# Performance work log

Hardware: AMD Instinct MI355X
Metric: run time of the kernel (lower is better)

## Reference

```python
import jax, jax.numpy as jnp
import numpy as np

NEG_INF = -1e20

def setup_inputs() -> dict:
    key = jax.random.key(0)
    kq, kk, kv, km = jax.random.split(key, 4)
    B, S, H, D = 2, 2048, 16, 64
    queries = jax.random.normal(kq, (B, S, H, D), dtype=jnp.float32)
    keys = jax.random.normal(kk, (B, S, H, D), dtype=jnp.float32)
    values = jax.random.normal(kv, (B, S, H, D), dtype=jnp.float32)
    mask = jax.random.randint(km, (B, 1, 1, S), 0, 2, dtype=jnp.int32)
    return {"queries": queries, "keys": keys, "values": values, "mask": mask}

def reference(queries, keys, values, mask):
    # scores: [B, H, Q, K]
    dk = keys.shape[-1]
    scores = jnp.einsum('bqhd,bkhd->bhqk', queries, keys) / jnp.sqrt(jnp.asarray(dk, queries.dtype))
    scores = jnp.where(mask == 0, jnp.asarray(NEG_INF, scores.dtype), scores)
    attn = jax.nn.softmax(scores, axis=-1)
    # dropout p=0.0 (eval): identity
    out = jnp.einsum('bhqv,bvhd->bqhd', attn, values)
    return out
```

## Files before the change

### kernel.cpp

```cpp
#include <hip/hip_runtime.h>
#include <hip/hip_bf16.h>

#define S_LEN 2048
#define NH 16
#define HD 64

typedef __attribute__((ext_vector_type(8))) __bf16 bf16x8;
typedef __attribute__((ext_vector_type(16))) float f32x16;

#define QSCALE 0.1803368801111204f

static __device__ __forceinline__ ushort f2bf(float f) {
    unsigned int u = __float_as_uint(f);
    u += 0x7fffu + ((u >> 16) & 1u);
    return (ushort)(u >> 16);
}

static __device__ __forceinline__ void gload16(const void* g, void* l) {
    __builtin_amdgcn_global_load_lds(
        (const __attribute__((address_space(1))) unsigned int*)g,
        (__attribute__((address_space(3))) unsigned int*)l, 16, 0, 0);
}
static __device__ __forceinline__ void gload4(const void* g, void* l) {
    __builtin_amdgcn_global_load_lds(
        (const __attribute__((address_space(1))) unsigned int*)g,
        (__attribute__((address_space(3))) unsigned int*)l, 4, 0, 0);
}

static __device__ __forceinline__ unsigned cvtpk_bf16(float lo, float hi) {
    unsigned r;
    asm("v_cvt_pk_bf16_f32 %0, %1, %2" : "=v"(r) : "v"(lo), "v"(hi));
    return r;
}
static __device__ __forceinline__ float exp2_fast(float x) {
    float r;
    asm("v_exp_f32 %0, %1" : "=v"(r) : "v"(x));
    return r;
}

__global__ __launch_bounds__(256) void prep_k_kernel(const float* __restrict__ in,
                                                     ushort* __restrict__ out) {
    unsigned t = blockIdx.x * 256u + threadIdx.x;
    unsigned o = t & 7u;
    unsigned s = (t >> 3) & 2047u;
    unsigned bh = t >> 14;
    unsigned b = bh >> 4, h = bh & 15u;
    const float* src = in + (((size_t)(b * S_LEN) + s) * NH + h) * HD + o * 8;
    float4 x = *(const float4*)src;
    float4 y = *(const float4*)(src + 4);
    union { ushort u[8]; uint4 q; } fu;
    fu.u[0] = f2bf(x.x); fu.u[1] = f2bf(x.y); fu.u[2] = f2bf(x.z); fu.u[3] = f2bf(x.w);
    fu.u[4] = f2bf(y.x); fu.u[5] = f2bf(y.y); fu.u[6] = f2bf(y.z); fu.u[7] = f2bf(y.w);
    unsigned kt = s >> 6, kh = (s >> 5) & 1u, kl = s & 31u;
    unsigned dchunk = o >> 1, ho = o & 1u;
    size_t ci = (((size_t)(bh * 32u + kt) * 2u + kh) * 4u + dchunk) * 64u + kl + 32u * ho;
    *(uint4*)(out + ci * 8u) = fu.q;
}

__global__ __launch_bounds__(256) void prep_v_kernel(const float* __restrict__ in,
                                                     ushort* __restrict__ out) {
    __shared__ float T[64][68];
    const unsigned tid = threadIdx.x;
    const unsigned kt = blockIdx.x, bh = blockIdx.y;
    const unsigned b = bh >> 4, h = bh & 15u;
#pragma unroll
    for (int i = 0; i < 4; ++i) {
        unsigned idx = tid + i * 256u;
        unsigned sl = idx >> 4, d4 = (idx & 15u) * 4u;
        float4 v = *(const float4*)(in + (((size_t)(b * S_LEN) + kt * 64u + sl) * NH + h) * HD + d4);
        *(float4*)&T[sl][d4] = v;
    }
    __syncthreads();
#pragma unroll
    for (int it = 0; it < 2; ++it) {
        unsigned ct = tid + it * 256u;
        unsigned l = ct & 63u, sub = ct >> 6;
        unsigned nt = sub & 1u, c = (sub >> 1) & 1u, kh = sub >> 2;
        unsigned d = (l & 31u) + 32u * nt;
        unsigned kb = kh * 32u + c * 16u + (l >> 5) * 8u;
        union { ushort u[8]; uint4 q; } fu;
#pragma unroll
        for (int j = 0; j < 8; ++j) fu.u[j] = f2bf(T[kb + j][d]);
        *(uint4*)(out + ((size_t)(bh * 32u + kt) * 8u + sub) * 512u + l * 8u) = fu.q;
    }
}

struct TileMem {
    ushort K[2][2][4096];
    ushort V[2][2][4096];
    int    mb[2][2][64];
};
struct CombMem {
    float ob[4][32][64];
    float lsb[4][64];
    float rls[4][32];
};
union SMemU { TileMem s; CombMem c; };

__global__ __launch_bounds__(512, 4) void attn_kernel(const float* __restrict__ Qp,
                                                      const ushort* __restrict__ Kws,
                                                      const ushort* __restrict__ Vws,
                                                      const int* __restrict__ maskp,
                                                      float* __restrict__ outp) {
    __shared__ __align__(16) SMemU sm;

    const unsigned tid = threadIdx.x;
    const unsigned wid = tid >> 6;
    const unsigned lane = tid & 63u;
    const unsigned l31 = lane & 31u;
    const unsigned hi = lane >> 5;
    const unsigned qsub = wid & 3u;
    const unsigned kgrp = wid >> 2;

    const unsigned bh = blockIdx.y;
    const unsigned b = bh >> 4, h = bh & 15u;
    const unsigned q0 = blockIdx.x * 128u + qsub * 32u;

    bf16x8 qf[4];
    {
        const float* qb = Qp + (((size_t)(b * S_LEN) + q0 + l31) * NH + h) * HD + hi * 8u;
#pragma unroll
        for (int dc = 0; dc < 4; ++dc) {
            float4 x = *(const float4*)(qb + dc * 16);
            float4 y = *(const float4*)(qb + dc * 16 + 4);
            union { ushort u[8]; bf16x8 v; } fu;
            fu.u[0] = f2bf(x.x * QSCALE); fu.u[1] = f2bf(x.y * QSCALE);
            fu.u[2] = f2bf(x.z * QSCALE); fu.u[3] = f2bf(x.w * QSCALE);
            fu.u[4] = f2bf(y.x * QSCALE); fu.u[5] = f2bf(y.y * QSCALE);
            fu.u[6] = f2bf(y.z * QSCALE); fu.u[7] = f2bf(y.w * QSCALE);
            qf[dc] = fu.v;
        }
    }

    f32x16 oacc0 = {0,0,0,0,0,0,0,0,0,0,0,0,0,0,0,0};
    f32x16 oacc1 = {0,0,0,0,0,0,0,0,0,0,0,0,0,0,0,0};
    float ls0 = 0.f, ls1 = 0.f, ls2 = 0.f, ls3 = 0.f;

    const char* kgp = (const char*)Kws + (size_t)bh * 262144u
                    + ((size_t)kgrp * 131072u) + (2u * qsub) * 1024u + lane * 16u;
    const char* vgp = (const char*)Vws + (size_t)bh * 262144u
                    + ((size_t)kgrp * 131072u) + (2u * qsub) * 1024u + lane * 16u;
    const int* mgp = maskp + (size_t)b * S_LEN + kgrp * 1024u + lane;

    ushort* klb = &sm.s.K[kgrp][0][2u * qsub * 512u];
    ushort* vlb = &sm.s.V[kgrp][0][2u * qsub * 512u];
    int*    mlb = &sm.s.mb[kgrp][0][0];
    const ushort* krd = &sm.s.K[kgrp][0][0];
    const ushort* vrd = &sm.s.V[kgrp][0][0];

#define STAGE(I, PB) do {                                                      \
    const size_t toff = (size_t)(I) * 8192u;                                   \
    gload16(kgp + toff,          klb + (PB) * 4096u);                          \
    gload16(kgp + toff + 1024u,  klb + (PB) * 4096u + 512u);                   \
    gload16(vgp + toff,          vlb + (PB) * 4096u);                          \
    gload16(vgp + toff + 1024u,  vlb + (PB) * 4096u + 512u);                   \
    if (qsub == 0) gload4(mgp + (I) * 64, mlb + (PB) * 64u);                   \
  } while (0)

    STAGE(0, 0u);
    asm volatile("s_waitcnt vmcnt(0)" ::: "memory");
    __syncthreads();

    unsigned pb = 0;
    for (int i = 0; i < 16; ++i) {
        if (i < 15) STAGE(i + 1, pb ^ 1u);
        const ushort* kr = krd + pb * 4096u;
        const ushort* vr = vrd + pb * 4096u;
        const int*    mr = mlb + pb * 64u;

#pragma unroll
        for (int kh = 0; kh < 2; ++kh) {
            bf16x8 kf[4];
#pragma unroll
            for (int dc = 0; dc < 4; ++dc)
                kf[dc] = *(const bf16x8*)&kr[(kh * 4 + dc) * 512u + lane * 8u];

            f32x16 s = {0,0,0,0,0,0,0,0,0,0,0,0,0,0,0,0};
            __builtin_amdgcn_s_setprio(1);
#pragma unroll
            for (int dc = 0; dc < 4; ++dc)
                s = __builtin_amdgcn_mfma_f32_32x32x16_bf16(kf[dc], qf[dc], s, 0, 0, 0);
            __builtin_amdgcn_s_setprio(0);

            float p[16];
#pragma unroll
            for (int r1 = 0; r1 < 4; ++r1) {
                int mv[4];
                *(int4*)mv = *(const int4*)&mr[kh * 32 + r1 * 8 + hi * 4];
#pragma unroll
                for (int r0 = 0; r0 < 4; ++r0) {
                    const int reg = r1 * 4 + r0;
                    float t = mv[r0] ? s[reg] : -1e30f;
                    p[reg] = exp2_fast(t);
                }
                ls0 += p[r1 * 4 + 0]; ls1 += p[r1 * 4 + 1];
                ls2 += p[r1 * 4 + 2]; ls3 += p[r1 * 4 + 3];
            }

#pragma unroll
            for (int c = 0; c < 2; ++c) {
                unsigned a0 = cvtpk_bf16(p[8 * c + 0], p[8 * c + 1]);
                unsigned a1 = cvtpk_bf16(p[8 * c + 2], p[8 * c + 3]);
                unsigned b0 = cvtpk_bf16(p[8 * c + 4], p[8 * c + 5]);
                unsigned b1 = cvtpk_bf16(p[8 * c + 6], p[8 * c + 7]);
                asm("v_permlane32_swap_b32 %0, %1" : "+v"(a0), "+v"(b0));
                asm("v_permlane32_swap_b32 %0, %1" : "+v"(a1), "+v"(b1));
                union { unsigned w[4]; bf16x8 v; } pa;
                pa.w[0] = a0; pa.w[1] = a1; pa.w[2] = b0; pa.w[3] = b1;
                bf16x8 vf0 = *(const bf16x8*)&vr[((kh * 2 + c) * 2 + 0) * 512u + lane * 8u];
                bf16x8 vf1 = *(const bf16x8*)&vr[((kh * 2 + c) * 2 + 1) * 512u + lane * 8u];
                __builtin_amdgcn_s_setprio(1);
                oacc0 = __builtin_amdgcn_mfma_f32_32x32x16_bf16(pa.v, vf0, oacc0, 0, 0, 0);
                oacc1 = __builtin_amdgcn_mfma_f32_32x32x16_bf16(pa.v, vf1, oacc1, 0, 0, 0);
                __builtin_amdgcn_s_setprio(0);
            }
        }
        asm volatile("s_waitcnt vmcnt(0)" ::: "memory");
        __syncthreads();
        pb ^= 1u;
    }
#undef STAGE

    float lsum = (ls0 + ls1) + (ls2 + ls3);
    lsum += __shfl_xor(lsum, 32);

    if (kgrp == 1) {
#pragma unroll
        for (int r = 0; r < 16; ++r) {
            sm.c.ob[qsub][r][lane]      = oacc0[r];
            sm.c.ob[qsub][16 + r][lane] = oacc1[r];
        }
        sm.c.lsb[qsub][lane] = lsum;
    }
    __syncthreads();
    if (kgrp == 0) {
        lsum += sm.c.lsb[qsub][lane];
#pragma unroll
        for (int r = 0; r < 16; ++r) {
            oacc0[r] += sm.c.ob[qsub][r][lane];
            oacc1[r] += sm.c.ob[qsub][16 + r][lane];
        }
        if (hi == 0) sm.c.rls[qsub][l31] = 1.0f / lsum;
#pragma unroll
        for (int r1 = 0; r1 < 4; ++r1) {
#pragma unroll
            for (int r0 = 0; r0 < 4; ++r0) {
                const int reg = r1 * 4 + r0;
                const unsigned q = r0 + 8u * r1 + 4u * hi;
                const float rr = sm.c.rls[qsub][q];
                float* ob = outp + (((size_t)(b * S_LEN) + q0 + q) * NH + h) * HD + l31;
                ob[0]  = oacc0[reg] * rr;
                ob[32] = oacc1[reg] * rr;
            }
        }
    }
}

extern "C" void kernel_launch(void* const* d_in, const int* in_sizes, int n_in,
                              void* d_out, int out_size, void* d_ws, size_t ws_size,
                              hipStream_t stream) {
    const float* Qp = (const float*)d_in[0];
    const float* Kp = (const float*)d_in[1];
    const float* Vp = (const float*)d_in[2];
    const int* maskp = (const int*)d_in[3];
    float* outp = (float*)d_out;

    ushort* Kws = (ushort*)d_ws;
    ushort* Vws = Kws + (size_t)2 * NH * S_LEN * HD;

    hipLaunchKernelGGL(prep_k_kernel, dim3(2048), dim3(256), 0, stream, Kp, Kws);
    hipLaunchKernelGGL(prep_v_kernel, dim3(32, 32), dim3(256), 0, stream, Vp, Vws);
    hipLaunchKernelGGL(attn_kernel, dim3(S_LEN / 128, 32), dim3(512), 0, stream,
                       Qp, Kws, Vws, maskp, outp);
}
```

Measured before the change: 64.16 us.

## Software-pipeline QK and softmax, compute row sums via MFMA, preload mask once

Restructures the inner loop so the second half-tile's QK MFMAs are issued between the first half's exp and its PV MFMAs, overlapping VALU work with matrix work. The row-sum accumulation moves from VALU adds plus a cross-lane shuffle to an extra MFMA against a vector of ones. The row sums then come out already in the output accumulator layout, so the shared-memory reciprocal broadcast is no longer needed. The whole mask row is loaded into LDS once instead of per tile. In exchange it adds 50% more PV MFMA work, raises accumulator register pressure, and sums bf16-rounded probabilities, which changes numerics slightly.

```diff
diff --git a/kernel.cpp b/kernel.cpp
--- a/kernel.cpp
+++ b/kernel.cpp
@@ -88,12 +88,11 @@
 struct TileMem {
     ushort K[2][2][4096];
     ushort V[2][2][4096];
-    int    mb[2][2][64];
+    int    mk[2][1024];
 };
 struct CombMem {
     float ob[4][32][64];
-    float lsb[4][64];
-    float rls[4][32];
+    float ls2[4][16][64];
 };
 union SMemU { TileMem s; CombMem c; };
 
@@ -132,19 +131,25 @@
         }
     }
 
+    bf16x8 one8;
+    {
+        union { ushort u[8]; bf16x8 v; } ou;
+#pragma unroll
+        for (int j = 0; j < 8; ++j) ou.u[j] = 0x3F80;
+        one8 = ou.v;
+    }
+
     f32x16 oacc0 = {0,0,0,0,0,0,0,0,0,0,0,0,0,0,0,0};
     f32x16 oacc1 = {0,0,0,0,0,0,0,0,0,0,0,0,0,0,0,0};
-    float ls0 = 0.f, ls1 = 0.f, ls2 = 0.f, ls3 = 0.f;
+    f32x16 oacc2 = {0,0,0,0,0,0,0,0,0,0,0,0,0,0,0,0};
 
     const char* kgp = (const char*)Kws + (size_t)bh * 262144u
                     + ((size_t)kgrp * 131072u) + (2u * qsub) * 1024u + lane * 16u;
     const char* vgp = (const char*)Vws + (size_t)bh * 262144u
                     + ((size_t)kgrp * 131072u) + (2u * qsub) * 1024u + lane * 16u;
-    const int* mgp = maskp + (size_t)b * S_LEN + kgrp * 1024u + lane;
 
     ushort* klb = &sm.s.K[kgrp][0][2u * qsub * 512u];
     ushort* vlb = &sm.s.V[kgrp][0][2u * qsub * 512u];
-    int*    mlb = &sm.s.mb[kgrp][0][0];
     const ushort* krd = &sm.s.K[kgrp][0][0];
     const ushort* vrd = &sm.s.V[kgrp][0][0];
 
@@ -154,9 +159,14 @@
     gload16(kgp + toff + 1024u,  klb + (PB) * 4096u + 512u);                   \
     gload16(vgp + toff,          vlb + (PB) * 4096u);                          \
     gload16(vgp + toff + 1024u,  vlb + (PB) * 4096u + 512u);                   \
-    if (qsub == 0) gload4(mgp + (I) * 64, mlb + (PB) * 64u);                   \
   } while (0)
 
+    {
+        const int* mgp = maskp + (size_t)b * S_LEN + kgrp * 1024u + qsub * 256u + lane;
+#pragma unroll
+        for (int j = 0; j < 4; ++j)
+            gload4(mgp + j * 64, &sm.s.mk[kgrp][qsub * 256u + j * 64u]);
+    }
     STAGE(0, 0u);
     asm volatile("s_waitcnt vmcnt(0)" ::: "memory");
     __syncthreads();
@@ -166,88 +176,120 @@
         if (i < 15) STAGE(i + 1, pb ^ 1u);
         const ushort* kr = krd + pb * 4096u;
         const ushort* vr = vrd + pb * 4096u;
-        const int*    mr = mlb + pb * 64u;
-
-#pragma unroll
-        for (int kh = 0; kh < 2; ++kh) {
-            bf16x8 kf[4];
-#pragma unroll
-            for (int dc = 0; dc < 4; ++dc)
-                kf[dc] = *(const bf16x8*)&kr[(kh * 4 + dc) * 512u + lane * 8u];
-
-            f32x16 s = {0,0,0,0,0,0,0,0,0,0,0,0,0,0,0,0};
+        const int*    mr = &sm.s.mk[kgrp][(unsigned)i * 64u];
+
+        bf16x8 kfa[4];
+#pragma unroll
+        for (int dc = 0; dc < 4; ++dc)
+            kfa[dc] = *(const bf16x8*)&kr[dc * 512u + lane * 8u];
+        f32x16 s0 = {0,0,0,0,0,0,0,0,0,0,0,0,0,0,0,0};
+        __builtin_amdgcn_s_setprio(1);
+#pragma unroll
+        for (int dc = 0; dc < 4; ++dc)
+            s0 = __builtin_amdgcn_mfma_f32_32x32x16_bf16(kfa[dc], qf[dc], s0, 0, 0, 0);
+        __builtin_amdgcn_s_setprio(0);
+
+        float p[16];
+#pragma unroll
+        for (int r1 = 0; r1 < 4; ++r1) {
+            int mv[4];
+            *(int4*)mv = *(const int4*)&mr[r1 * 8 + hi * 4];
+#pragma unroll
+            for (int r0 = 0; r0 < 4; ++r0) {
+                const int reg = r1 * 4 + r0;
+                p[reg] = exp2_fast(mv[r0] ? s0[reg] : -1e30f);
+            }
+        }
+
+        bf16x8 kfb[4];
+#pragma unroll
+        for (int dc = 0; dc < 4; ++dc)
+            kfb[dc] = *(const bf16x8*)&kr[(4 + dc) * 512u + lane * 8u];
+        f32x16 s1 = {0,0,0,0,0,0,0,0,0,0,0,0,0,0,0,0};
+        __builtin_amdgcn_s_setprio(1);
+#pragma unroll
+        for (int dc = 0; dc < 4; ++dc)
+            s1 = __builtin_amdgcn_mfma_f32_32x32x16_bf16(kfb[dc], qf[dc], s1, 0, 0, 0);
+        __builtin_amdgcn_s_setprio(0);
+
+#pragma unroll
+        for (int c = 0; c < 2; ++c) {
+            unsigned a0 = cvtpk_bf16(p[8 * c + 0], p[8 * c + 1]);
+            unsigned a1 = cvtpk_bf16(p[8 * c + 2], p[8 * c + 3]);
+            unsigned b0 = cvtpk_bf16(p[8 * c + 4], p[8 * c + 5]);
+            unsigned b1 = cvtpk_bf16(p[8 * c + 6], p[8 * c + 7]);
+            asm("v_permlane32_swap_b32 %0, %1" : "+v"(a0), "+v"(b0));
+            asm("v_permlane32_swap_b32 %0, %1" : "+v"(a1), "+v"(b1));
+            union { unsigned w[4]; bf16x8 v; } pa;
+            pa.w[0] = a0; pa.w[1] = a1; pa.w[2] = b0; pa.w[3] = b1;
+            bf16x8 vf0 = *(const bf16x8*)&vr[(c * 2 + 0) * 512u + lane * 8u];
+            bf16x8 vf1 = *(const bf16x8*)&vr[(c * 2 + 1) * 512u + lane * 8u];
             __builtin_amdgcn_s_setprio(1);
-#pragma unroll
-            for (int dc = 0; dc < 4; ++dc)
-                s = __builtin_amdgcn_mfma_f32_32x32x16_bf16(kf[dc], qf[dc], s, 0, 0, 0);
+            oacc0 = __builtin_amdgcn_mfma_f32_32x32x16_bf16(pa.v, vf0, oacc0, 0, 0, 0);
+            oacc1 = __builtin_amdgcn_mfma_f32_32x32x16_bf16(pa.v, vf1, oacc1, 0, 0, 0);
+            oacc2 = __builtin_amdgcn_mfma_f32_32x32x16_bf16(pa.v, one8, oacc2, 0, 0, 0);
             __builtin_amdgcn_s_setprio(0);
-
-            float p[16];
-#pragma unroll
-            for (int r1 = 0; r1 < 4; ++r1) {
-                int mv[4];
-                *(int4*)mv = *(const int4*)&mr[kh * 32 + r1 * 8 + hi * 4];
-#pragma unroll
-                for (int r0 = 0; r0 < 4; ++r0) {
-                    const int reg = r1 * 4 + r0;
-                    float t = mv[r0] ? s[reg] : -1e30f;
-                    p[reg] = exp2_fast(t);
-                }
-                ls0 += p[r1 * 4 + 0]; ls1 += p[r1 * 4 + 1];
-                ls2 += p[r1 * 4 + 2]; ls3 += p[r1 * 4 + 3];
+        }
+
+#pragma unroll
+        for (int r1 = 0; r1 < 4; ++r1) {
+            int mv[4];
+            *(int4*)mv = *(const int4*)&mr[32 + r1 * 8 + hi * 4];
+#pragma unroll
+            for (int r0 = 0; r0 < 4; ++r0) {
+                const int reg = r1 * 4 + r0;
+                p[reg] = exp2_fast(mv[r0] ? s1[reg] : -1e30f);
             }
-
-#pragma unroll
-            for (int c = 0; c < 2; ++c) {
-                unsigned a0 = cvtpk_bf16(p[8 * c + 0], p[8 * c + 1]);
-                unsigned a1 = cvtpk_bf16(p[8 * c + 2], p[8 * c + 3]);
-                unsigned b0 = cvtpk_bf16(p[8 * c + 4], p[8 * c + 5]);
-                unsigned b1 = cvtpk_bf16(p[8 * c + 6], p[8 * c + 7]);
-                asm("v_permlane32_swap_b32 %0, %1" : "+v"(a0), "+v"(b0));
-                asm("v_permlane32_swap_b32 %0, %1" : "+v"(a1), "+v"(b1));
-                union { unsigned w[4]; bf16x8 v; } pa;
-                pa.w[0] = a0; pa.w[1] = a1; pa.w[2] = b0; pa.w[3] = b1;
-                bf16x8 vf0 = *(const bf16x8*)&vr[((kh * 2 + c) * 2 + 0) * 512u + lane * 8u];
-                bf16x8 vf1 = *(const bf16x8*)&vr[((kh * 2 + c) * 2 + 1) * 512u + lane * 8u];
-                __builtin_amdgcn_s_setprio(1);
-                oacc0 = __builtin_amdgcn_mfma_f32_32x32x16_bf16(pa.v, vf0, oacc0, 0, 0, 0);
-                oacc1 = __builtin_amdgcn_mfma_f32_32x32x16_bf16(pa.v, vf1, oacc1, 0, 0, 0);
-                __builtin_amdgcn_s_setprio(0);
-            }
-        }
+        }
+
+#pragma unroll
+        for (int c = 0; c < 2; ++c) {
+            unsigned a0 = cvtpk_bf16(p[8 * c + 0], p[8 * c + 1]);
+            unsigned a1 = cvtpk_bf16(p[8 * c + 2], p[8 * c + 3]);
+            unsigned b0 = cvtpk_bf16(p[8 * c + 4], p[8 * c + 5]);
+            unsigned b1 = cvtpk_bf16(p[8 * c + 6], p[8 * c + 7]);
+            asm("v_permlane32_swap_b32 %0, %1" : "+v"(a0), "+v"(b0));
+            asm("v_permlane32_swap_b32 %0, %1" : "+v"(a1), "+v"(b1));
+            union { unsigned w[4]; bf16x8 v; } pa;
+            pa.w[0] = a0; pa.w[1] = a1; pa.w[2] = b0; pa.w[3] = b1;
+            bf16x8 vf0 = *(const bf16x8*)&vr[((2 + c) * 2 + 0) * 512u + lane * 8u];
+            bf16x8 vf1 = *(const bf16x8*)&vr[((2 + c) * 2 + 1) * 512u + lane * 8u];
+            __builtin_amdgcn_s_setprio(1);
+            oacc0 = __builtin_amdgcn_mfma_f32_32x32x16_bf16(pa.v, vf0, oacc0, 0, 0, 0);
+            oacc1 = __builtin_amdgcn_mfma_f32_32x32x16_bf16(pa.v, vf1, oacc1, 0, 0, 0);
+            oacc2 = __builtin_amdgcn_mfma_f32_32x32x16_bf16(pa.v, one8, oacc2, 0, 0, 0);
+            __builtin_amdgcn_s_setprio(0);
+        }
+
         asm volatile("s_waitcnt vmcnt(0)" ::: "memory");
         __syncthreads();
         pb ^= 1u;
     }
 #undef STAGE
 
-    float lsum = (ls0 + ls1) + (ls2 + ls3);
-    lsum += __shfl_xor(lsum, 32);
-
     if (kgrp == 1) {
 #pragma unroll
         for (int r = 0; r < 16; ++r) {
             sm.c.ob[qsub][r][lane]      = oacc0[r];
             sm.c.ob[qsub][16 + r][lane] = oacc1[r];
-        }
-        sm.c.lsb[qsub][lane] = lsum;
+            sm.c.ls2[qsub][r][lane]     = oacc2[r];
+        }
     }
     __syncthreads();
     if (kgrp == 0) {
-        lsum += sm.c.lsb[qsub][lane];
 #pragma unroll
         for (int r = 0; r < 16; ++r) {
             oacc0[r] += sm.c.ob[qsub][r][lane];
             oacc1[r] += sm.c.ob[qsub][16 + r][lane];
-        }
-        if (hi == 0) sm.c.rls[qsub][l31] = 1.0f / lsum;
+            oacc2[r] += sm.c.ls2[qsub][r][lane];
+        }
 #pragma unroll
         for (int r1 = 0; r1 < 4; ++r1) {
 #pragma unroll
             for (int r0 = 0; r0 < 4; ++r0) {
                 const int reg = r1 * 4 + r0;
                 const unsigned q = r0 + 8u * r1 + 4u * hi;
-                const float rr = sm.c.rls[qsub][q];
+                const float rr = 1.0f / oacc2[reg];
                 float* ob = outp + (((size_t)(b * S_LEN) + q0 + q) * NH + h) * HD + l31;
                 ob[0]  = oacc0[reg] * rr;
                 ob[32] = oacc1[reg] * rr;
```

After: 66.49 us. 3.6% more time.

## Use triple-buffered 32-key tiles with prefetch depth two and preloaded mask

Applied to the files above, without the earlier changes.

Changes the K/V staging from double-buffered 64-key tiles to triple-buffered 32-key tiles, prefetching two tiles ahead and waiting with vmcnt(2) instead of draining all loads each iteration. The whole per-group mask slice is loaded into LDS once up front rather than per tile. The aim is to hide global load latency behind MFMA work and cut the per-iteration mask loads. In exchange it doubles the number of iterations and barriers, and it relies on a raw s_barrier with partial vmcnt waits being enough to order the LDS-direct loads.

```diff
diff --git a/kernel.cpp b/kernel.cpp
--- a/kernel.cpp
+++ b/kernel.cpp
@@ -86,9 +86,9 @@
 }
 
 struct TileMem {
-    ushort K[2][2][4096];
-    ushort V[2][2][4096];
-    int    mb[2][2][64];
+    ushort K[2][3][2048];
+    ushort V[2][3][2048];
+    int    mk[2][1024];
 };
 struct CombMem {
     float ob[4][32][64];
@@ -136,88 +136,89 @@
     f32x16 oacc1 = {0,0,0,0,0,0,0,0,0,0,0,0,0,0,0,0};
     float ls0 = 0.f, ls1 = 0.f, ls2 = 0.f, ls3 = 0.f;
 
-    const char* kgp = (const char*)Kws + (size_t)bh * 262144u
-                    + ((size_t)kgrp * 131072u) + (2u * qsub) * 1024u + lane * 16u;
-    const char* vgp = (const char*)Vws + (size_t)bh * 262144u
-                    + ((size_t)kgrp * 131072u) + (2u * qsub) * 1024u + lane * 16u;
-    const int* mgp = maskp + (size_t)b * S_LEN + kgrp * 1024u + lane;
-
-    ushort* klb = &sm.s.K[kgrp][0][2u * qsub * 512u];
-    ushort* vlb = &sm.s.V[kgrp][0][2u * qsub * 512u];
-    int*    mlb = &sm.s.mb[kgrp][0][0];
+    const char* kgp = (const char*)(Kws + (size_t)bh * 131072u
+                    + (size_t)kgrp * 65536u) + qsub * 1024u + lane * 16u;
+    const char* vgp = (const char*)(Vws + (size_t)bh * 131072u
+                    + (size_t)kgrp * 65536u) + qsub * 1024u + lane * 16u;
+
+    ushort* klb = &sm.s.K[kgrp][0][qsub * 512u];
+    ushort* vlb = &sm.s.V[kgrp][0][qsub * 512u];
     const ushort* krd = &sm.s.K[kgrp][0][0];
     const ushort* vrd = &sm.s.V[kgrp][0][0];
 
-#define STAGE(I, PB) do {                                                      \
-    const size_t toff = (size_t)(I) * 8192u;                                   \
-    gload16(kgp + toff,          klb + (PB) * 4096u);                          \
-    gload16(kgp + toff + 1024u,  klb + (PB) * 4096u + 512u);                   \
-    gload16(vgp + toff,          vlb + (PB) * 4096u);                          \
-    gload16(vgp + toff + 1024u,  vlb + (PB) * 4096u + 512u);                   \
-    if (qsub == 0) gload4(mgp + (I) * 64, mlb + (PB) * 64u);                   \
+#define STAGE(T, BUF) do {                                                     \
+    const size_t toff = (size_t)(T) * 4096u;                                   \
+    gload16(kgp + toff, klb + (BUF) * 2048u);                                  \
+    gload16(vgp + toff, vlb + (BUF) * 2048u);                                  \
   } while (0)
 
+    {
+        const int* mgp = maskp + (size_t)b * S_LEN + kgrp * 1024u + qsub * 256u + lane;
+#pragma unroll
+        for (int j = 0; j < 4; ++j)
+            gload4(mgp + j * 64, &sm.s.mk[kgrp][qsub * 256u + j * 64u]);
+    }
     STAGE(0, 0u);
-    asm volatile("s_waitcnt vmcnt(0)" ::: "memory");
-    __syncthreads();
-
-    unsigned pb = 0;
-    for (int i = 0; i < 16; ++i) {
-        if (i < 15) STAGE(i + 1, pb ^ 1u);
-        const ushort* kr = krd + pb * 4096u;
-        const ushort* vr = vrd + pb * 4096u;
-        const int*    mr = mlb + pb * 64u;
-
-#pragma unroll
-        for (int kh = 0; kh < 2; ++kh) {
-            bf16x8 kf[4];
-#pragma unroll
-            for (int dc = 0; dc < 4; ++dc)
-                kf[dc] = *(const bf16x8*)&kr[(kh * 4 + dc) * 512u + lane * 8u];
-
-            f32x16 s = {0,0,0,0,0,0,0,0,0,0,0,0,0,0,0,0};
+    STAGE(1, 1u);
+    asm volatile("s_waitcnt vmcnt(2)" ::: "memory");
+    __builtin_amdgcn_s_barrier();
+
+    unsigned cur = 0u, st = 2u;
+    for (int t = 0; t < 32; ++t) {
+        if (t < 30) STAGE(t + 2, st);
+        const ushort* kr = krd + cur * 2048u;
+        const ushort* vr = vrd + cur * 2048u;
+        const int*    mr = &sm.s.mk[kgrp][(unsigned)t * 32u];
+
+        bf16x8 kf[4];
+#pragma unroll
+        for (int dc = 0; dc < 4; ++dc)
+            kf[dc] = *(const bf16x8*)&kr[dc * 512u + lane * 8u];
+
+        f32x16 s = {0,0,0,0,0,0,0,0,0,0,0,0,0,0,0,0};
+        __builtin_amdgcn_s_setprio(1);
+#pragma unroll
+        for (int dc = 0; dc < 4; ++dc)
+            s = __builtin_amdgcn_mfma_f32_32x32x16_bf16(kf[dc], qf[dc], s, 0, 0, 0);
+        __builtin_amdgcn_s_setprio(0);
+
+        float p[16];
+#pragma unroll
+        for (int r1 = 0; r1 < 4; ++r1) {
+            int mv[4];
+            *(int4*)mv = *(const int4*)&mr[r1 * 8 + hi * 4];
+#pragma unroll
+            for (int r0 = 0; r0 < 4; ++r0) {
+                const int reg = r1 * 4 + r0;
+                p[reg] = exp2_fast(mv[r0] ? s[reg] : -1e30f);
+            }
+            ls0 += p[r1 * 4 + 0]; ls1 += p[r1 * 4 + 1];
+            ls2 += p[r1 * 4 + 2]; ls3 += p[r1 * 4 + 3];
+        }
+
+#pragma unroll
+        for (int c = 0; c < 2; ++c) {
+            unsigned a0 = cvtpk_bf16(p[8 * c + 0], p[8 * c + 1]);
+            unsigned a1 = cvtpk_bf16(p[8 * c + 2], p[8 * c + 3]);
+            unsigned b0 = cvtpk_bf16(p[8 * c + 4], p[8 * c + 5]);
+            unsigned b1 = cvtpk_bf16(p[8 * c + 6], p[8 * c + 7]);
+            asm("v_permlane32_swap_b32 %0, %1" : "+v"(a0), "+v"(b0));
+            asm("v_permlane32_swap_b32 %0, %1" : "+v"(a1), "+v"(b1));
+            union { unsigned w[4]; bf16x8 v; } pa;
+            pa.w[0] = a0; pa.w[1] = a1; pa.w[2] = b0; pa.w[3] = b1;
+            bf16x8 vf0 = *(const bf16x8*)&vr[(c * 2 + 0) * 512u + lane * 8u];
+            bf16x8 vf1 = *(const bf16x8*)&vr[(c * 2 + 1) * 512u + lane * 8u];
             __builtin_amdgcn_s_setprio(1);
-#pragma unroll
-            for (int dc = 0; dc < 4; ++dc)
-                s = __builtin_amdgcn_mfma_f32_32x32x16_bf16(kf[dc], qf[dc], s, 0, 0, 0);
+            oacc0 = __builtin_amdgcn_mfma_f32_32x32x16_bf16(pa.v, vf0, oacc0, 0, 0, 0);
+            oacc1 = __builtin_amdgcn_mfma_f32_32x32x16_bf16(pa.v, vf1, oacc1, 0, 0, 0);
             __builtin_amdgcn_s_setprio(0);
-
-            float p[16];
-#pragma unroll
-            for (int r1 = 0; r1 < 4; ++r1) {
-                int mv[4];
-                *(int4*)mv = *(const int4*)&mr[kh * 32 + r1 * 8 + hi * 4];
-#pragma unroll
-                for (int r0 = 0; r0 < 4; ++r0) {
-                    const int reg = r1 * 4 + r0;
-                    float t = mv[r0] ? s[reg] : -1e30f;
-                    p[reg] = exp2_fast(t);
-                }
-                ls0 += p[r1 * 4 + 0]; ls1 += p[r1 * 4 + 1];
-                ls2 += p[r1 * 4 + 2]; ls3 += p[r1 * 4 + 3];
-            }
-
-#pragma unroll
-            for (int c = 0; c < 2; ++c) {
-                unsigned a0 = cvtpk_bf16(p[8 * c + 0], p[8 * c + 1]);
-                unsigned a1 = cvtpk_bf16(p[8 * c + 2], p[8 * c + 3]);
-                unsigned b0 = cvtpk_bf16(p[8 * c + 4], p[8 * c + 5]);
-                unsigned b1 = cvtpk_bf16(p[8 * c + 6], p[8 * c + 7]);
-                asm("v_permlane32_swap_b32 %0, %1" : "+v"(a0), "+v"(b0));
-                asm("v_permlane32_swap_b32 %0, %1" : "+v"(a1), "+v"(b1));
-                union { unsigned w[4]; bf16x8 v; } pa;
-                pa.w[0] = a0; pa.w[1] = a1; pa.w[2] = b0; pa.w[3] = b1;
-                bf16x8 vf0 = *(const bf16x8*)&vr[((kh * 2 + c) * 2 + 0) * 512u + lane * 8u];
-                bf16x8 vf1 = *(const bf16x8*)&vr[((kh * 2 + c) * 2 + 1) * 512u + lane * 8u];
-                __builtin_amdgcn_s_setprio(1);
-                oacc0 = __builtin_amdgcn_mfma_f32_32x32x16_bf16(pa.v, vf0, oacc0, 0, 0, 0);
-                oacc1 = __builtin_amdgcn_mfma_f32_32x32x16_bf16(pa.v, vf1, oacc1, 0, 0, 0);
-                __builtin_amdgcn_s_setprio(0);
-            }
-        }
-        asm volatile("s_waitcnt vmcnt(0)" ::: "memory");
-        __syncthreads();
-        pb ^= 1u;
+        }
+
+        if (t < 30) asm volatile("s_waitcnt vmcnt(2)" ::: "memory");
+        else        asm volatile("s_waitcnt vmcnt(0)" ::: "memory");
+        __builtin_amdgcn_s_barrier();
+        cur = (cur == 2u) ? 0u : cur + 1u;
+        st  = (st  == 2u) ? 0u : st  + 1u;
     }
 #undef STAGE
 
```

Result: no change. 65.21 us (+1.6%).
